# Kernel optimization log

Hardware: AMD Instinct MI355X
Metric: run time of the kernel (lower is better)

## Reference

```python
import jax, jax.numpy as jnp
import numpy as np

EPS = 1e-7  # keras.backend.epsilon()


def setup_inputs() -> dict:
    key = jax.random.key(0)
    k1, k2 = jax.random.split(key)
    B, S, D = 8, 1024, 768
    # scale down: module exponentiates raw dot products with no max-subtraction
    input_a = jax.random.normal(k1, (B, S, D), dtype=jnp.float32) * 0.05
    input_mask = jax.random.randint(k2, (B, S), 0, 2, dtype=jnp.int32)
    return {"input_a": input_a, "input_mask": input_mask}


def reference(input_a, input_mask):
    # e = exp(Q K^T) with Q = K = input_a, attend_type='dot' (no scaling)
    e = jnp.exp(jnp.einsum('bsd,btd->bst', input_a, input_a))  # [B,S,S]
    m = input_mask.astype(input_a.dtype)
    e = e * m[:, :, None] * m[:, None, :]  # mask rows and cols
    e = e / (jnp.sum(e, axis=-1, keepdims=True) + EPS)  # renormalize
    attend = jnp.einsum('bst,btd->bsd', e, input_a)  # V = input_a
    return attend
```

## Files before the change

### kernel.cpp

```cpp
#include <hip/hip_runtime.h>
#include <cstdint>
#include <cstddef>

#define BATCH 8
#define SEQ 1024
#define DIM 768
#define EPS_K 1e-7f

typedef __bf16 bf16x8 __attribute__((ext_vector_type(8)));
typedef float f32x4 __attribute__((ext_vector_type(4)));

__device__ __forceinline__ uint16_t f2bf(float f) {
  union { float f; uint32_t u; } v; v.f = f;
  uint32_t u = v.u;
  u += 0x7FFFu + ((u >> 16) & 1u);
  return (uint16_t)(u >> 16);
}

__device__ __forceinline__ void gload16(const void* g, void* l) {
  __builtin_amdgcn_global_load_lds(
      (const __attribute__((address_space(1))) uint32_t*)g,
      (__attribute__((address_space(3))) uint32_t*)l, 16, 0, 0);
}

__global__ __launch_bounds__(256) void convert_kernel(const float* __restrict__ A,
                                                      uint16_t* __restrict__ ab,
                                                      uint16_t* __restrict__ at) {
  const int b  = blockIdx.z;
  const int s0 = blockIdx.y * 64;
  const int d0 = blockIdx.x * 64;
  __shared__ uint16_t tl[64][66];
  const int c  = threadIdx.x & 63;
  const int r0 = threadIdx.x >> 6;
  const float* Ab = A + (size_t)b * SEQ * DIM;
  uint16_t* abb = ab + (size_t)b * SEQ * DIM;
#pragma unroll
  for (int i = 0; i < 16; ++i) {
    int r = r0 + i * 4;
    uint16_t h = f2bf(Ab[(size_t)(s0 + r) * DIM + d0 + c]);
    abb[(size_t)(s0 + r) * DIM + d0 + c] = h;
    tl[r][c] = h;
  }
  __syncthreads();
  uint16_t* atb = at + (size_t)b * DIM * SEQ;
#pragma unroll
  for (int i = 0; i < 16; ++i) {
    int r = r0 + i * 4;
    atb[(size_t)(d0 + r) * SEQ + s0 + c] = tl[c][r];
  }
}

__global__ __launch_bounds__(256) void scores_kernel(const uint16_t* __restrict__ ab,
                                                     const int* __restrict__ mask,
                                                     uint16_t* __restrict__ P) {
  const int b    = blockIdx.x & 7;
  const int tile = blockIdx.x >> 3;
  const int s0   = (tile >> 3) * 128;
  const int t0   = (tile & 7) * 128;

  const int tid  = threadIdx.x;
  const int lane = tid & 63;
  const int wid  = tid >> 6;
  const int wr   = wid >> 1;
  const int wc   = wid & 1;

  __shared__ uint16_t ldsQ[2][128 * 32];
  __shared__ uint16_t ldsK[2][128 * 32];
  __shared__ float mrow[128];
  __shared__ float mcol[128];

  if (tid < 128)        mrow[tid]       = (float)mask[b * SEQ + s0 + tid];
  else                  mcol[tid - 128] = (float)mask[b * SEQ + t0 + (tid - 128)];

  const uint16_t* aQ = ab + (size_t)b * SEQ * DIM + (size_t)s0 * DIM;
  const uint16_t* aK = ab + (size_t)b * SEQ * DIM + (size_t)t0 * DIM;

  const int sr = (tid * 8) >> 5;
  const int sc = (tid * 8) & 31;
#define STAGE(buf, k0)                                                         \
  do {                                                                         \
    int _i0 = tid * 8, _i1 = (256 + tid) * 8;                                  \
    gload16(aQ + (size_t)sr * DIM + (k0) + sc,        &ldsQ[buf][_i0]);        \
    gload16(aQ + (size_t)(sr + 64) * DIM + (k0) + sc, &ldsQ[buf][_i1]);        \
    gload16(aK + (size_t)sr * DIM + (k0) + sc,        &ldsK[buf][_i0]);        \
    gload16(aK + (size_t)(sr + 64) * DIM + (k0) + sc, &ldsK[buf][_i1]);        \
  } while (0)

  f32x4 acc[4][4];
#pragma unroll
  for (int m = 0; m < 4; ++m)
#pragma unroll
    for (int n = 0; n < 4; ++n) acc[m][n] = f32x4{0.f, 0.f, 0.f, 0.f};

  STAGE(0, 0);
  __syncthreads();

  const int rowQ = wr * 64 + (lane & 15);
  const int rowK = wc * 64 + (lane & 15);
  const int kch  = (lane >> 4) * 8;

  int cur = 0;
  for (int k0 = 0; k0 < DIM; k0 += 32) {
    if (k0 + 32 < DIM) STAGE(cur ^ 1, k0 + 32);

    bf16x8 qf[4], kf[4];
#pragma unroll
    for (int m = 0; m < 4; ++m) qf[m] = *(const bf16x8*)&ldsQ[cur][(rowQ + m * 16) * 32 + kch];
#pragma unroll
    for (int n = 0; n < 4; ++n) kf[n] = *(const bf16x8*)&ldsK[cur][(rowK + n * 16) * 32 + kch];
#pragma unroll
    for (int m = 0; m < 4; ++m)
#pragma unroll
      for (int n = 0; n < 4; ++n)
        acc[m][n] = __builtin_amdgcn_mfma_f32_16x16x32_bf16(qf[m], kf[n], acc[m][n], 0, 0, 0);

    __syncthreads();
    cur ^= 1;
  }
#undef STAGE

  uint16_t* Pb = P + (size_t)b * SEQ * SEQ;
#pragma unroll
  for (int m = 0; m < 4; ++m) {
    const int qb = wr * 64 + m * 16 + (lane >> 4) * 4;
#pragma unroll
    for (int n = 0; n < 4; ++n) {
      const int tloc = wc * 64 + n * 16 + (lane & 15);
      const float mc = mcol[tloc];
#pragma unroll
      for (int j = 0; j < 4; ++j) {
        float e = __expf(acc[m][n][j]) * mrow[qb + j] * mc;
        Pb[(size_t)(s0 + qb + j) * SEQ + t0 + tloc] = f2bf(e);
      }
    }
  }
}

__global__ __launch_bounds__(256) void out_kernel(const uint16_t* __restrict__ P,
                                                  const uint16_t* __restrict__ at,
                                                  float* __restrict__ out) {
  const int b    = blockIdx.x & 7;
  const int tile = blockIdx.x >> 3;
  const int q0   = (tile / 6) * 128;
  const int d0   = (tile % 6) * 128;

  const int tid  = threadIdx.x;
  const int lane = tid & 63;
  const int wid  = tid >> 6;
  const int wr   = wid >> 1;
  const int wc   = wid & 1;

  __shared__ uint16_t ldsP[2][128 * 32];
  __shared__ uint16_t ldsA[2][128 * 32];

  const uint16_t* Pb = P  + (size_t)b * SEQ * SEQ + (size_t)q0 * SEQ;
  const uint16_t* Ab = at + (size_t)b * DIM * SEQ + (size_t)d0 * SEQ;

  const int sr = (tid * 8) >> 5;
  const int sc = (tid * 8) & 31;
#define STAGE(buf, k0)                                                         \
  do {                                                                         \
    int _i0 = tid * 8, _i1 = (256 + tid) * 8;                                  \
    gload16(Pb + (size_t)sr * SEQ + (k0) + sc,        &ldsP[buf][_i0]);        \
    gload16(Pb + (size_t)(sr + 64) * SEQ + (k0) + sc, &ldsP[buf][_i1]);        \
    gload16(Ab + (size_t)sr * SEQ + (k0) + sc,        &ldsA[buf][_i0]);        \
    gload16(Ab + (size_t)(sr + 64) * SEQ + (k0) + sc, &ldsA[buf][_i1]);        \
  } while (0)

  f32x4 acc[4][4];
  f32x4 accd[4];
#pragma unroll
  for (int m = 0; m < 4; ++m) {
    accd[m] = f32x4{0.f, 0.f, 0.f, 0.f};
#pragma unroll
    for (int n = 0; n < 4; ++n) acc[m][n] = f32x4{0.f, 0.f, 0.f, 0.f};
  }

  bf16x8 onesf;
#pragma unroll
  for (int i = 0; i < 8; ++i) onesf[i] = (__bf16)1.0f;

  STAGE(0, 0);
  __syncthreads();

  const int rowP = wr * 64 + (lane & 15);
  const int rowA = wc * 64 + (lane & 15);
  const int kch  = (lane >> 4) * 8;

  int cur = 0;
  for (int k0 = 0; k0 < SEQ; k0 += 32) {
    if (k0 + 32 < SEQ) STAGE(cur ^ 1, k0 + 32);

    bf16x8 pf[4], af[4];
#pragma unroll
    for (int m = 0; m < 4; ++m) pf[m] = *(const bf16x8*)&ldsP[cur][(rowP + m * 16) * 32 + kch];
#pragma unroll
    for (int n = 0; n < 4; ++n) af[n] = *(const bf16x8*)&ldsA[cur][(rowA + n * 16) * 32 + kch];
#pragma unroll
    for (int m = 0; m < 4; ++m) {
#pragma unroll
      for (int n = 0; n < 4; ++n)
        acc[m][n] = __builtin_amdgcn_mfma_f32_16x16x32_bf16(pf[m], af[n], acc[m][n], 0, 0, 0);
      accd[m] = __builtin_amdgcn_mfma_f32_16x16x32_bf16(pf[m], onesf, accd[m], 0, 0, 0);
    }

    __syncthreads();
    cur ^= 1;
  }
#undef STAGE

  float* ob = out + (size_t)b * SEQ * DIM;
#pragma unroll
  for (int m = 0; m < 4; ++m) {
#pragma unroll
    for (int j = 0; j < 4; ++j) {
      const int ql = wr * 64 + m * 16 + (lane >> 4) * 4 + j;
      const float sc2 = 1.0f / (accd[m][j] + EPS_K);
#pragma unroll
      for (int n = 0; n < 4; ++n) {
        const int dl = d0 + wc * 64 + n * 16 + (lane & 15);
        ob[(size_t)(q0 + ql) * DIM + dl] = acc[m][n][j] * sc2;
      }
    }
  }
}

extern "C" void kernel_launch(void* const* d_in, const int* in_sizes, int n_in,
                              void* d_out, int out_size, void* d_ws, size_t ws_size,
                              hipStream_t stream) {
  (void)in_sizes; (void)n_in; (void)out_size; (void)ws_size;
  const float* A    = (const float*)d_in[0];
  const int*   mask = (const int*)d_in[1];
  float*       out  = (float*)d_out;

  char* ws = (char*)d_ws;
  const size_t NB_AB = (size_t)BATCH * SEQ * DIM * 2;
  const size_t NB_AT = NB_AB;
  uint16_t* ab = (uint16_t*)(ws);
  uint16_t* at = (uint16_t*)(ws + NB_AB);
  uint16_t* P  = (uint16_t*)(ws + NB_AB + NB_AT);

  dim3 blk(256);
  convert_kernel<<<dim3(DIM / 64, SEQ / 64, BATCH), blk, 0, stream>>>(A, ab, at);
  scores_kernel<<<dim3(64 * BATCH), blk, 0, stream>>>(ab, mask, P);
  out_kernel<<<dim3(48 * BATCH), blk, 0, stream>>>(P, at, out);
}
```

Baseline: 118.6 us.

## Switch GEMMs to 32x32x16 MFMA with XOR-swizzled LDS and vectorized conversion

Both GEMM kernels move from 16x16x32 to 32x32x16 bf16 MFMA tiles, which cuts the number of LDS fragment reads per MFMA. The LDS staging layout gains an XOR swizzle to avoid bank conflicts. The conversion/transpose kernel now uses float4 loads and 16-byte vector stores instead of scalar accesses. The epilogue store pattern changes with the new accumulator layout, and the strided 2-byte P stores remain uncoalesced.

```diff
diff --git a/kernel.cpp b/kernel.cpp
--- a/kernel.cpp
+++ b/kernel.cpp
@@ -8,7 +8,10 @@
 #define EPS_K 1e-7f
 
 typedef __bf16 bf16x8 __attribute__((ext_vector_type(8)));
-typedef float f32x4 __attribute__((ext_vector_type(4)));
+typedef float f32x16 __attribute__((ext_vector_type(16)));
+typedef uint16_t u16x8 __attribute__((ext_vector_type(8)));
+
+#define MFMA32(a, b, c) __builtin_amdgcn_mfma_f32_32x32x16_bf16((a), (b), (c), 0, 0, 0)
 
 __device__ __forceinline__ uint16_t f2bf(float f) {
   union { float f; uint32_t u; } v; v.f = f;
@@ -29,26 +32,33 @@
   const int b  = blockIdx.z;
   const int s0 = blockIdx.y * 64;
   const int d0 = blockIdx.x * 64;
-  __shared__ uint16_t tl[64][66];
-  const int c  = threadIdx.x & 63;
-  const int r0 = threadIdx.x >> 6;
-  const float* Ab = A + (size_t)b * SEQ * DIM;
-  uint16_t* abb = ab + (size_t)b * SEQ * DIM;
-#pragma unroll
-  for (int i = 0; i < 16; ++i) {
-    int r = r0 + i * 4;
-    uint16_t h = f2bf(Ab[(size_t)(s0 + r) * DIM + d0 + c]);
-    abb[(size_t)(s0 + r) * DIM + d0 + c] = h;
-    tl[r][c] = h;
+  __shared__ uint16_t tl[64][80];
+  const int tid = threadIdx.x;
+#pragma unroll
+  for (int i = 0; i < 2; ++i) {
+    const int sl = (tid >> 3) + i * 32;
+    const int ch = tid & 7;
+    const float* src = A + ((size_t)b * SEQ + s0 + sl) * DIM + d0 + ch * 8;
+    float4 f0 = *(const float4*)src;
+    float4 f1 = *(const float4*)(src + 4);
+    u16x8 h;
+    h[0] = f2bf(f0.x); h[1] = f2bf(f0.y); h[2] = f2bf(f0.z); h[3] = f2bf(f0.w);
+    h[4] = f2bf(f1.x); h[5] = f2bf(f1.y); h[6] = f2bf(f1.z); h[7] = f2bf(f1.w);
+    *(u16x8*)&ab[((size_t)b * SEQ + s0 + sl) * DIM + d0 + ch * 8] = h;
+    *(u16x8*)&tl[sl][ch * 8] = h;
   }
   __syncthreads();
-  uint16_t* atb = at + (size_t)b * DIM * SEQ;
-#pragma unroll
-  for (int i = 0; i < 16; ++i) {
-    int r = r0 + i * 4;
-    atb[(size_t)(d0 + r) * SEQ + s0 + c] = tl[c][r];
-  }
-}
+  const int dl = tid >> 2;
+#pragma unroll
+  for (int i = 0; i < 2; ++i) {
+    const int sc = (tid & 3) + i * 4;
+    u16x8 h;
+#pragma unroll
+    for (int e = 0; e < 8; ++e) h[e] = tl[sc * 8 + e][dl];
+    *(u16x8*)&at[((size_t)b * DIM + d0 + dl) * SEQ + s0 + sc * 8] = h;
+  }
+}
+
 
 __global__ __launch_bounds__(256) void scores_kernel(const uint16_t* __restrict__ ab,
                                                      const int* __restrict__ mask,
@@ -60,77 +70,92 @@
 
   const int tid  = threadIdx.x;
   const int lane = tid & 63;
+  const int l31  = lane & 31;
+  const int lhi  = lane >> 5;
   const int wid  = tid >> 6;
   const int wr   = wid >> 1;
   const int wc   = wid & 1;
 
-  __shared__ uint16_t ldsQ[2][128 * 32];
-  __shared__ uint16_t ldsK[2][128 * 32];
+  __shared__ __align__(16) uint16_t lQ[2][128 * 32];
+  __shared__ __align__(16) uint16_t lK[2][128 * 32];
   __shared__ float mrow[128];
   __shared__ float mcol[128];
 
   if (tid < 128)        mrow[tid]       = (float)mask[b * SEQ + s0 + tid];
   else                  mcol[tid - 128] = (float)mask[b * SEQ + t0 + (tid - 128)];
 
-  const uint16_t* aQ = ab + (size_t)b * SEQ * DIM + (size_t)s0 * DIM;
-  const uint16_t* aK = ab + (size_t)b * SEQ * DIM + (size_t)t0 * DIM;
-
-  const int sr = (tid * 8) >> 5;
-  const int sc = (tid * 8) & 31;
-#define STAGE(buf, k0)                                                         \
-  do {                                                                         \
-    int _i0 = tid * 8, _i1 = (256 + tid) * 8;                                  \
-    gload16(aQ + (size_t)sr * DIM + (k0) + sc,        &ldsQ[buf][_i0]);        \
-    gload16(aQ + (size_t)(sr + 64) * DIM + (k0) + sc, &ldsQ[buf][_i1]);        \
-    gload16(aK + (size_t)sr * DIM + (k0) + sc,        &ldsK[buf][_i0]);        \
-    gload16(aK + (size_t)(sr + 64) * DIM + (k0) + sc, &ldsK[buf][_i1]);        \
-  } while (0)
-
-  f32x4 acc[4][4];
-#pragma unroll
-  for (int m = 0; m < 4; ++m)
-#pragma unroll
-    for (int n = 0; n < 4; ++n) acc[m][n] = f32x4{0.f, 0.f, 0.f, 0.f};
-
-  STAGE(0, 0);
+  const uint16_t* gQ = ab + ((size_t)b * SEQ + s0) * DIM;
+  const uint16_t* gK = ab + ((size_t)b * SEQ + t0) * DIM;
+
+  const int strow = tid >> 2;
+  const int schx  = (((tid & 3) ^ ((tid >> 3) & 3)) << 3);
+  const int sdst  = tid * 8;
+#define STG(L, G, LDG, buf, k0)                                                \
+  { gload16(G + (size_t)strow * (LDG) + (k0) + schx, &L[buf][sdst]);           \
+    gload16(G + (size_t)(strow + 64) * (LDG) + (k0) + schx,                    \
+            &L[buf][sdst + 2048]); }
+
+  f32x16 acc[2][2];
+#pragma unroll
+  for (int m = 0; m < 2; ++m)
+#pragma unroll
+    for (int n = 0; n < 2; ++n)
+#pragma unroll
+      for (int r = 0; r < 16; ++r) acc[m][n][r] = 0.f;
+
+  int offQ[2][2], offK[2][2];
+#pragma unroll
+  for (int m = 0; m < 2; ++m) {
+    const int rQ = wr * 64 + m * 32 + l31;
+    const int rK = wc * 64 + m * 32 + l31;
+#pragma unroll
+    for (int kk = 0; kk < 2; ++kk) {
+      offQ[m][kk] = rQ * 32 + (((kk << 1) + lhi) ^ ((rQ >> 1) & 3)) * 8;
+      offK[m][kk] = rK * 32 + (((kk << 1) + lhi) ^ ((rK >> 1) & 3)) * 8;
+    }
+  }
+
+  STG(lQ, gQ, DIM, 0, 0); STG(lK, gK, DIM, 0, 0);
   __syncthreads();
 
-  const int rowQ = wr * 64 + (lane & 15);
-  const int rowK = wc * 64 + (lane & 15);
-  const int kch  = (lane >> 4) * 8;
-
+  const int NT = DIM / 32;
   int cur = 0;
-  for (int k0 = 0; k0 < DIM; k0 += 32) {
-    if (k0 + 32 < DIM) STAGE(cur ^ 1, k0 + 32);
-
-    bf16x8 qf[4], kf[4];
-#pragma unroll
-    for (int m = 0; m < 4; ++m) qf[m] = *(const bf16x8*)&ldsQ[cur][(rowQ + m * 16) * 32 + kch];
-#pragma unroll
-    for (int n = 0; n < 4; ++n) kf[n] = *(const bf16x8*)&ldsK[cur][(rowK + n * 16) * 32 + kch];
-#pragma unroll
-    for (int m = 0; m < 4; ++m)
-#pragma unroll
-      for (int n = 0; n < 4; ++n)
-        acc[m][n] = __builtin_amdgcn_mfma_f32_16x16x32_bf16(qf[m], kf[n], acc[m][n], 0, 0, 0);
+  for (int t = 0; t < NT; ++t) {
+    const int nx = cur ^ 1;
+    if (t + 1 < NT) { STG(lQ, gQ, DIM, nx, (t + 1) * 32); STG(lK, gK, DIM, nx, (t + 1) * 32); }
+
+    bf16x8 qf[2][2], kf[2][2];
+#pragma unroll
+    for (int m = 0; m < 2; ++m)
+#pragma unroll
+      for (int kk = 0; kk < 2; ++kk) {
+        qf[m][kk] = *(const bf16x8*)&lQ[cur][offQ[m][kk]];
+        kf[m][kk] = *(const bf16x8*)&lK[cur][offK[m][kk]];
+      }
+#pragma unroll
+    for (int kk = 0; kk < 2; ++kk)
+#pragma unroll
+      for (int m = 0; m < 2; ++m)
+#pragma unroll
+        for (int n = 0; n < 2; ++n)
+          acc[m][n] = MFMA32(qf[m][kk], kf[n][kk], acc[m][n]);
 
     __syncthreads();
     cur ^= 1;
   }
-#undef STAGE
 
   uint16_t* Pb = P + (size_t)b * SEQ * SEQ;
 #pragma unroll
-  for (int m = 0; m < 4; ++m) {
-    const int qb = wr * 64 + m * 16 + (lane >> 4) * 4;
-#pragma unroll
-    for (int n = 0; n < 4; ++n) {
-      const int tloc = wc * 64 + n * 16 + (lane & 15);
-      const float mc = mcol[tloc];
-#pragma unroll
-      for (int j = 0; j < 4; ++j) {
-        float e = __expf(acc[m][n][j]) * mrow[qb + j] * mc;
-        Pb[(size_t)(s0 + qb + j) * SEQ + t0 + tloc] = f2bf(e);
+  for (int m = 0; m < 2; ++m) {
+#pragma unroll
+    for (int n = 0; n < 2; ++n) {
+      const int cl = wc * 64 + n * 32 + l31;
+      const float mc = mcol[cl];
+#pragma unroll
+      for (int r = 0; r < 16; ++r) {
+        const int rl = wr * 64 + m * 32 + (r & 3) + 8 * (r >> 2) + 4 * lhi;
+        float e = __expf(acc[m][n][r]) * mrow[rl] * mc;
+        Pb[(size_t)(s0 + rl) * SEQ + t0 + cl] = f2bf(e);
       }
     }
   }
@@ -146,84 +171,96 @@
 
   const int tid  = threadIdx.x;
   const int lane = tid & 63;
+  const int l31  = lane & 31;
+  const int lhi  = lane >> 5;
   const int wid  = tid >> 6;
   const int wr   = wid >> 1;
   const int wc   = wid & 1;
 
-  __shared__ uint16_t ldsP[2][128 * 32];
-  __shared__ uint16_t ldsA[2][128 * 32];
-
-  const uint16_t* Pb = P  + (size_t)b * SEQ * SEQ + (size_t)q0 * SEQ;
-  const uint16_t* Ab = at + (size_t)b * DIM * SEQ + (size_t)d0 * SEQ;
-
-  const int sr = (tid * 8) >> 5;
-  const int sc = (tid * 8) & 31;
-#define STAGE(buf, k0)                                                         \
-  do {                                                                         \
-    int _i0 = tid * 8, _i1 = (256 + tid) * 8;                                  \
-    gload16(Pb + (size_t)sr * SEQ + (k0) + sc,        &ldsP[buf][_i0]);        \
-    gload16(Pb + (size_t)(sr + 64) * SEQ + (k0) + sc, &ldsP[buf][_i1]);        \
-    gload16(Ab + (size_t)sr * SEQ + (k0) + sc,        &ldsA[buf][_i0]);        \
-    gload16(Ab + (size_t)(sr + 64) * SEQ + (k0) + sc, &ldsA[buf][_i1]);        \
-  } while (0)
-
-  f32x4 acc[4][4];
-  f32x4 accd[4];
-#pragma unroll
-  for (int m = 0; m < 4; ++m) {
-    accd[m] = f32x4{0.f, 0.f, 0.f, 0.f};
-#pragma unroll
-    for (int n = 0; n < 4; ++n) acc[m][n] = f32x4{0.f, 0.f, 0.f, 0.f};
-  }
-
-  bf16x8 onesf;
-#pragma unroll
-  for (int i = 0; i < 8; ++i) onesf[i] = (__bf16)1.0f;
-
-  STAGE(0, 0);
+  __shared__ __align__(16) uint16_t lP[2][128 * 32];
+  __shared__ __align__(16) uint16_t lV[2][128 * 32];
+
+  const uint16_t* gP = P  + ((size_t)b * SEQ + q0) * SEQ;
+  const uint16_t* gV = at + ((size_t)b * DIM + d0) * SEQ;
+
+  const int strow = tid >> 2;
+  const int schx  = (((tid & 3) ^ ((tid >> 3) & 3)) << 3);
+  const int sdst  = tid * 8;
+
+  f32x16 acc[2][2];
+  f32x16 accd[2];
+#pragma unroll
+  for (int m = 0; m < 2; ++m) {
+#pragma unroll
+    for (int r = 0; r < 16; ++r) accd[m][r] = 0.f;
+#pragma unroll
+    for (int n = 0; n < 2; ++n)
+#pragma unroll
+      for (int r = 0; r < 16; ++r) acc[m][n][r] = 0.f;
+  }
+  bf16x8 ones;
+#pragma unroll
+  for (int i = 0; i < 8; ++i) ones[i] = (__bf16)1.0f;
+
+  int offP[2][2], offV[2][2];
+#pragma unroll
+  for (int m = 0; m < 2; ++m) {
+    const int rP = wr * 64 + m * 32 + l31;
+    const int rV = wc * 64 + m * 32 + l31;
+#pragma unroll
+    for (int kk = 0; kk < 2; ++kk) {
+      offP[m][kk] = rP * 32 + (((kk << 1) + lhi) ^ ((rP >> 1) & 3)) * 8;
+      offV[m][kk] = rV * 32 + (((kk << 1) + lhi) ^ ((rV >> 1) & 3)) * 8;
+    }
+  }
+
+  STG(lP, gP, SEQ, 0, 0); STG(lV, gV, SEQ, 0, 0);
   __syncthreads();
 
-  const int rowP = wr * 64 + (lane & 15);
-  const int rowA = wc * 64 + (lane & 15);
-  const int kch  = (lane >> 4) * 8;
-
+  const int NT = SEQ / 32;
   int cur = 0;
-  for (int k0 = 0; k0 < SEQ; k0 += 32) {
-    if (k0 + 32 < SEQ) STAGE(cur ^ 1, k0 + 32);
-
-    bf16x8 pf[4], af[4];
-#pragma unroll
-    for (int m = 0; m < 4; ++m) pf[m] = *(const bf16x8*)&ldsP[cur][(rowP + m * 16) * 32 + kch];
-#pragma unroll
-    for (int n = 0; n < 4; ++n) af[n] = *(const bf16x8*)&ldsA[cur][(rowA + n * 16) * 32 + kch];
-#pragma unroll
-    for (int m = 0; m < 4; ++m) {
-#pragma unroll
-      for (int n = 0; n < 4; ++n)
-        acc[m][n] = __builtin_amdgcn_mfma_f32_16x16x32_bf16(pf[m], af[n], acc[m][n], 0, 0, 0);
-      accd[m] = __builtin_amdgcn_mfma_f32_16x16x32_bf16(pf[m], onesf, accd[m], 0, 0, 0);
-    }
+  for (int t = 0; t < NT; ++t) {
+    const int nx = cur ^ 1;
+    if (t + 1 < NT) { STG(lP, gP, SEQ, nx, (t + 1) * 32); STG(lV, gV, SEQ, nx, (t + 1) * 32); }
+
+    bf16x8 pf[2][2], vf[2][2];
+#pragma unroll
+    for (int m = 0; m < 2; ++m)
+#pragma unroll
+      for (int kk = 0; kk < 2; ++kk) {
+        pf[m][kk] = *(const bf16x8*)&lP[cur][offP[m][kk]];
+        vf[m][kk] = *(const bf16x8*)&lV[cur][offV[m][kk]];
+      }
+#pragma unroll
+    for (int kk = 0; kk < 2; ++kk)
+#pragma unroll
+      for (int m = 0; m < 2; ++m) {
+#pragma unroll
+        for (int n = 0; n < 2; ++n)
+          acc[m][n] = MFMA32(pf[m][kk], vf[n][kk], acc[m][n]);
+        accd[m] = MFMA32(pf[m][kk], ones, accd[m]);
+      }
 
     __syncthreads();
     cur ^= 1;
   }
-#undef STAGE
 
   float* ob = out + (size_t)b * SEQ * DIM;
 #pragma unroll
-  for (int m = 0; m < 4; ++m) {
-#pragma unroll
-    for (int j = 0; j < 4; ++j) {
-      const int ql = wr * 64 + m * 16 + (lane >> 4) * 4 + j;
-      const float sc2 = 1.0f / (accd[m][j] + EPS_K);
-#pragma unroll
-      for (int n = 0; n < 4; ++n) {
-        const int dl = d0 + wc * 64 + n * 16 + (lane & 15);
-        ob[(size_t)(q0 + ql) * DIM + dl] = acc[m][n][j] * sc2;
-      }
-    }
-  }
-}
+  for (int m = 0; m < 2; ++m) {
+#pragma unroll
+    for (int r = 0; r < 16; ++r) {
+      const int rl = wr * 64 + m * 32 + (r & 3) + 8 * (r >> 2) + 4 * lhi;
+      const float sc = 1.0f / (accd[m][r] + EPS_K);
+#pragma unroll
+      for (int n = 0; n < 2; ++n) {
+        const int d = d0 + wc * 64 + n * 32 + l31;
+        ob[(size_t)(q0 + rl) * DIM + d] = acc[m][n][r] * sc;
+      }
+    }
+  }
+}
+#undef STG
 
 extern "C" void kernel_launch(void* const* d_in, const int* in_sizes, int n_in,
                               void* d_out, int out_size, void* d_ws, size_t ws_size,
@@ -240,8 +277,7 @@
   uint16_t* at = (uint16_t*)(ws + NB_AB);
   uint16_t* P  = (uint16_t*)(ws + NB_AB + NB_AT);
 
-  dim3 blk(256);
-  convert_kernel<<<dim3(DIM / 64, SEQ / 64, BATCH), blk, 0, stream>>>(A, ab, at);
-  scores_kernel<<<dim3(64 * BATCH), blk, 0, stream>>>(ab, mask, P);
-  out_kernel<<<dim3(48 * BATCH), blk, 0, stream>>>(P, at, out);
-}
+  convert_kernel<<<dim3(DIM / 64, SEQ / 64, BATCH), dim3(256), 0, stream>>>(A, ab, at);
+  scores_kernel<<<dim3(64 * BATCH), dim3(256), 0, stream>>>(ab, mask, P);
+  out_kernel<<<dim3(48 * BATCH), dim3(256), 0, stream>>>(P, at, out);
+}
```

New measurement: 126.7 us. +6.8%, slower.
